# Optimization experiments

Hardware: AMD Instinct MI355X
Metric: run time of the kernel (lower is better)

Reference implementation:

```python
import jax, jax.numpy as jnp
import numpy as np

NUM_EXPERTS = 64
TOP_K = 2
NOISE_STD = 1.0
LOAD_BALANCE_WEIGHT = 0.01
NOISE_KEY = jax.random.fold_in(jax.random.key(0), 12345)


def setup_inputs() -> dict:
    key = jax.random.key(0)
    k1, k2, k3 = jax.random.split(key, 3)
    B, S, D = 4, 4096, 1024
    x = jax.random.normal(k1, (B, S, D), dtype=jnp.float32)
    W_gate = jax.random.normal(k2, (NUM_EXPERTS, D), dtype=jnp.float32) * (1.0 / np.sqrt(D))
    W_noise = jax.random.normal(k3, (NUM_EXPERTS, D), dtype=jnp.float32) * (1.0 / np.sqrt(D))
    return {"x": x, "W_gate": W_gate, "W_noise": W_noise}


def reference(x, W_gate, W_noise):
    # x: [B,S,D], W_gate/W_noise: [E,D] (torch Linear weight layout)
    clean_logits = jnp.einsum("bsd,ed->bse", x, W_gate)           # [B,S,E]
    noise_scale = jax.nn.softplus(jnp.einsum("bsd,ed->bse", x, W_noise))
    noise = jax.random.normal(NOISE_KEY, clean_logits.shape, clean_logits.dtype)
    logits = clean_logits + noise * noise_scale * NOISE_STD

    probs = jax.nn.softmax(logits, axis=-1)                        # [B,S,E]
    routing_weights, expert_indices = jax.lax.top_k(probs, TOP_K)  # [B,S,K]
    routing_weights = routing_weights / jnp.sum(routing_weights, axis=-1, keepdims=True)

    # Load-balance loss on clean logits
    B, S, E = clean_logits.shape
    num_tokens = B * S
    expert_mask = jax.nn.one_hot(expert_indices, E, dtype=jnp.float32).sum(axis=2)  # [B,S,E]
    tokens_per_expert = expert_mask.sum(axis=(0, 1))               # [E]
    fraction_tokens = tokens_per_expert / num_tokens
    router_probs = jax.nn.softmax(clean_logits, axis=-1)
    mean_router_prob = router_probs.mean(axis=(0, 1))              # [E]
    load_balance_loss = LOAD_BALANCE_WEIGHT * E * jnp.sum(fraction_tokens * mean_router_prob)

    noise_scale_mean = noise_scale.mean()
    return (routing_weights, expert_indices, load_balance_loss, router_probs, noise_scale_mean)
```

## Files before the change

kernel.cpp:

```cpp
#include <hip/hip_runtime.h>
#include <stdint.h>

#define TOKENS 16384
#define DDIM   1024
#define NEXP   64
#define NCOL   128
#define TB     32
#define NBLK   (TOKENS / TB)
#define NCH    (DDIM / 32)
#define NTILE  8
#define CPP    8

typedef __attribute__((ext_vector_type(8))) short bf16x8;
typedef __attribute__((ext_vector_type(4))) float f32x4;

__device__ ushort g_wf[3][NTILE][NCH][64][8];
__device__ float g_ps[NEXP];
__device__ float g_cnt[NEXP];
__device__ float g_spa[1];

__device__ inline ushort bf16rne(float f) {
  uint32_t u = __float_as_uint(f);
  return (ushort)((u + 0x7fffu + ((u >> 16) & 1u)) >> 16);
}
__device__ inline float bf16tof(ushort h) {
  return __uint_as_float(((uint32_t)h) << 16);
}
__device__ inline void split3(float v, ushort& h, ushort& m, ushort& l) {
  h = bf16rne(v);
  float r1 = v - bf16tof(h);
  m = bf16rne(r1);
  float r2 = r1 - bf16tof(m);
  l = bf16rne(r2);
}

struct U2 { uint32_t a, b; };

__host__ __device__ constexpr U2 tf2x32(uint32_t k0, uint32_t k1,
                                        uint32_t x0, uint32_t x1) {
  uint32_t ks[3] = {k0, k1, k0 ^ k1 ^ 0x1BD11BDAu};
  const uint32_t rot[2][4] = {{13u, 15u, 26u, 6u}, {17u, 29u, 16u, 24u}};
  x0 += ks[0]; x1 += ks[1];
  for (int d = 0; d < 5; ++d) {
    for (int j = 0; j < 4; ++j) {
      uint32_t r = rot[d & 1][j];
      x0 += x1;
      x1 = (x1 << r) | (x1 >> (32u - r));
      x1 ^= x0;
    }
    x0 += ks[(d + 1) % 3];
    x1 += ks[(d + 2) % 3] + (uint32_t)(d + 1);
  }
  return U2{x0, x1};
}

__device__ inline uint32_t noise_bits(uint32_t i) {
  constexpr U2 NK = tf2x32(0u, 0u, 0u, 12345u);
  U2 o = tf2x32(NK.a, NK.b, 0u, i);
  return o.a ^ o.b;
}

__device__ inline float xla_erfinv(float x) {
  float w = -log1pf(-x * x);
  float p;
  if (w < 5.0f) {
    w = w - 2.5f;
    p = 2.81022636e-08f;
    p = 3.43273939e-07f + p * w;
    p = -3.5233877e-06f + p * w;
    p = -4.39150654e-06f + p * w;
    p = 0.00021858087f + p * w;
    p = -0.00125372503f + p * w;
    p = -0.00417768164f + p * w;
    p = 0.246640727f + p * w;
    p = 1.50140941f + p * w;
  } else {
    w = sqrtf(w) - 3.0f;
    p = -0.000200214257f;
    p = 0.000100950558f + p * w;
    p = 0.00134934322f + p * w;
    p = -0.00367342844f + p * w;
    p = 0.00573950773f + p * w;
    p = -0.0076224613f + p * w;
    p = 0.00943887047f + p * w;
    p = 1.00167406f + p * w;
    p = 2.83297682f + p * w;
  }
  return p * x;
}

__device__ inline float noise_normal(uint32_t i) {
  uint32_t bits = noise_bits(i);
  float f = __uint_as_float((bits >> 9) | 0x3f800000u) - 1.0f;
  float u = f * 2.0f + (-0.99999994f);
  u = fmaxf(u, -0.99999994f);
  return 1.41421356237f * xla_erfinv(u);
}

__device__ inline float softplus_ref(float x) {
  return fmaxf(x, 0.0f) + log1pf(expf(-fabsf(x)));
}

__device__ inline float wave_max64(float v) {
  #pragma unroll
  for (int off = 32; off; off >>= 1) v = fmaxf(v, __shfl_xor(v, off, 64));
  return v;
}
__device__ inline float wave_sum64(float v) {
  #pragma unroll
  for (int off = 32; off; off >>= 1) v += __shfl_xor(v, off, 64);
  return v;
}
__device__ inline void wave_argmax64(float v, int idx, float& mv, int& mi) {
  float bv = v; int bi = idx;
  #pragma unroll
  for (int off = 32; off; off >>= 1) {
    float ov = __shfl_xor(bv, off, 64);
    int   oi = __shfl_xor(bi, off, 64);
    if (ov > bv || (ov == bv && oi < bi)) { bv = ov; bi = oi; }
  }
  mv = bv; mi = bi;
}

__global__ __launch_bounds__(64)
void wsplit_kernel(const float* __restrict__ wg, const float* __restrict__ wn) {
  const int ct   = blockIdx.x >> 5;
  const int kc   = blockIdx.x & 31;
  const int lane = threadIdx.x;
  const int col  = ct * 16 + (lane & 15);
  const int koff = kc * 32 + (lane >> 4) * 8;
  const float* src = (col < NEXP) ? (wg + (size_t)col * DDIM)
                                  : (wn + (size_t)(col - NEXP) * DDIM);
  const float4 v0 = *(const float4*)&src[koff];
  const float4 v1 = *(const float4*)&src[koff + 4];
  const float av[8] = {v0.x, v0.y, v0.z, v0.w, v1.x, v1.y, v1.z, v1.w};
  union BF8 { bf16x8 v; ushort u[8]; };
  BF8 H, M, L;
  #pragma unroll
  for (int j = 0; j < 8; ++j) {
    ushort h, m, l;
    split3(av[j], h, m, l);
    H.u[j] = h; M.u[j] = m; L.u[j] = l;
  }
  *(bf16x8*)&g_wf[0][ct][kc][lane][0] = H.v;
  *(bf16x8*)&g_wf[1][ct][kc][lane][0] = M.v;
  *(bf16x8*)&g_wf[2][ct][kc][lane][0] = L.v;

  if (blockIdx.x == 0) {
    g_ps[lane] = 0.0f; g_cnt[lane] = 0.0f;
    if (lane == 0) g_spa[0] = 0.0f;
  }
}

__global__ __launch_bounds__(512, 4)
void NoisyTopKRouter_57621281243491_kernel(
    const float* __restrict__ x, float* __restrict__ out) {
  __shared__ ushort ldsA[3][2][CPP][64][8];
  __shared__ float lds_logits[TB][NCOL + 4];
  __shared__ float lps[8][NEXP];
  __shared__ float lcb[8][NEXP];
  __shared__ float lspw[8];

  const int tid  = threadIdx.x;
  const int w    = tid >> 6;
  const int lane = tid & 63;
  const int tok0 = blockIdx.x * TB;

  const int srow = tid >> 4;
  const int skq  = tid & 15;
  const int stg  = srow >> 4;
  const int sfr  = srow & 15;
  const int sc   = skq >> 1;
  const int sl0  = ((skq & 1) * 2) * 16 + sfr;
  const int sl1  = ((skq & 1) * 2 + 1) * 16 + sfr;
  const float* sx = x + (size_t)(tok0 + srow) * DDIM + skq * 16;

  const int fr_row = lane & 15;
  const int fr_s   = lane >> 4;
  const ushort* wf = &g_wf[0][0][0][0][0];
  const int b0 = w * 16384 + lane * 8;
  #define PS 131072

  f32x4 acc0 = {0.f, 0.f, 0.f, 0.f};
  f32x4 acc1 = {0.f, 0.f, 0.f, 0.f};

  float4 xrA[4], xrB[4];

  #define SPLIT_PHASE(XR)                                                 \
    {                                                                     \
      union BF8 { bf16x8 v; ushort u[8]; };                               \
      BF8 H0, M0, L0, H1, M1, L1;                                         \
      const float a0v[8] = {XR[0].x, XR[0].y, XR[0].z, XR[0].w,           \
                            XR[1].x, XR[1].y, XR[1].z, XR[1].w};          \
      const float a1v[8] = {XR[2].x, XR[2].y, XR[2].z, XR[2].w,           \
                            XR[3].x, XR[3].y, XR[3].z, XR[3].w};          \
      _Pragma("unroll")                                                   \
      for (int j = 0; j < 8; ++j) {                                       \
        ushort h, m, l;                                                   \
        split3(a0v[j], h, m, l);                                          \
        H0.u[j] = h; M0.u[j] = m; L0.u[j] = l;                            \
        split3(a1v[j], h, m, l);                                          \
        H1.u[j] = h; M1.u[j] = m; L1.u[j] = l;                            \
      }                                                                   \
      *(bf16x8*)&ldsA[0][stg][sc][sl0][0] = H0.v;                         \
      *(bf16x8*)&ldsA[1][stg][sc][sl0][0] = M0.v;                         \
      *(bf16x8*)&ldsA[2][stg][sc][sl0][0] = L0.v;                         \
      *(bf16x8*)&ldsA[0][stg][sc][sl1][0] = H1.v;                         \
      *(bf16x8*)&ldsA[1][stg][sc][sl1][0] = M1.v;                         \
      *(bf16x8*)&ldsA[2][stg][sc][sl1][0] = L1.v;                         \
    }

  #define MFMA_PHASE(ph)                                                  \
    _Pragma("unroll 2")                                                   \
    for (int c = 0; c < CPP; ++c) {                                       \
      const bf16x8 Ah0 = *(const bf16x8*)&ldsA[0][0][c][lane][0];         \
      const bf16x8 Am0 = *(const bf16x8*)&ldsA[1][0][c][lane][0];         \
      const bf16x8 Al0 = *(const bf16x8*)&ldsA[2][0][c][lane][0];         \
      const bf16x8 Ah1 = *(const bf16x8*)&ldsA[0][1][c][lane][0];         \
      const bf16x8 Am1 = *(const bf16x8*)&ldsA[1][1][c][lane][0];         \
      const bf16x8 Al1 = *(const bf16x8*)&ldsA[2][1][c][lane][0];         \
      const int co = ((ph) * CPP + c) * 512;                              \
      const bf16x8 Bh = *(const bf16x8*)&wf[b0 + co];                     \
      const bf16x8 Bm = *(const bf16x8*)&wf[b0 + PS + co];                \
      const bf16x8 Bl = *(const bf16x8*)&wf[b0 + 2 * PS + co];            \
      acc0 = __builtin_amdgcn_mfma_f32_16x16x32_bf16(Ah0, Bh, acc0, 0, 0, 0); \
      acc0 = __builtin_amdgcn_mfma_f32_16x16x32_bf16(Ah0, Bm, acc0, 0, 0, 0); \
      acc0 = __builtin_amdgcn_mfma_f32_16x16x32_bf16(Am0, Bh, acc0, 0, 0, 0); \
      acc0 = __builtin_amdgcn_mfma_f32_16x16x32_bf16(Ah0, Bl, acc0, 0, 0, 0); \
      acc0 = __builtin_amdgcn_mfma_f32_16x16x32_bf16(Al0, Bh, acc0, 0, 0, 0); \
      acc0 = __builtin_amdgcn_mfma_f32_16x16x32_bf16(Am0, Bm, acc0, 0, 0, 0); \
      acc1 = __builtin_amdgcn_mfma_f32_16x16x32_bf16(Ah1, Bh, acc1, 0, 0, 0); \
      acc1 = __builtin_amdgcn_mfma_f32_16x16x32_bf16(Ah1, Bm, acc1, 0, 0, 0); \
      acc1 = __builtin_amdgcn_mfma_f32_16x16x32_bf16(Am1, Bh, acc1, 0, 0, 0); \
      acc1 = __builtin_amdgcn_mfma_f32_16x16x32_bf16(Ah1, Bl, acc1, 0, 0, 0); \
      acc1 = __builtin_amdgcn_mfma_f32_16x16x32_bf16(Al1, Bh, acc1, 0, 0, 0); \
      acc1 = __builtin_amdgcn_mfma_f32_16x16x32_bf16(Am1, Bm, acc1, 0, 0, 0); \
    }

  #pragma unroll
  for (int q = 0; q < 4; ++q) xrA[q] = *(const float4*)&sx[q * 4];

  SPLIT_PHASE(xrA);
  #pragma unroll
  for (int q = 0; q < 4; ++q) xrB[q] = *(const float4*)&sx[256 + q * 4];
  __syncthreads();
  MFMA_PHASE(0);
  __syncthreads();
  SPLIT_PHASE(xrB);
  #pragma unroll
  for (int q = 0; q < 4; ++q) xrA[q] = *(const float4*)&sx[512 + q * 4];
  __syncthreads();
  MFMA_PHASE(1);
  __syncthreads();
  SPLIT_PHASE(xrA);
  #pragma unroll
  for (int q = 0; q < 4; ++q) xrB[q] = *(const float4*)&sx[768 + q * 4];
  __syncthreads();
  MFMA_PHASE(2);
  __syncthreads();
  SPLIT_PHASE(xrB);
  __syncthreads();
  MFMA_PHASE(3);

  #undef SPLIT_PHASE
  #undef MFMA_PHASE
  #undef PS

  #pragma unroll
  for (int r = 0; r < 4; ++r) {
    lds_logits[4 * fr_s + r][w * 16 + fr_row]      = acc0[r];
    lds_logits[16 + 4 * fr_s + r][w * 16 + fr_row] = acc1[r];
  }
  __syncthreads();

  float* out_rw  = out;
  float* out_idx = out + 2 * TOKENS;
  float* out_rp  = out + 4 * TOKENS + 1;

  float ps_acc = 0.0f, sp_acc = 0.0f, c_acc = 0.0f;

  for (int it = 0; it < 4; ++it) {
    const int tl = w * 4 + it;
    const int t  = tok0 + tl;
    const float cl = lds_logits[tl][lane];
    const float nl = lds_logits[tl][NEXP + lane];

    const float m  = wave_max64(cl);
    const float v  = expf(cl - m);
    const float Z  = wave_sum64(v);
    const float rp = v / Z;
    out_rp[(size_t)t * NEXP + lane] = rp;
    ps_acc += rp;

    const float ns  = softplus_ref(nl);
    sp_acc += ns;
    const float noi = noise_normal((uint32_t)(t * NEXP + lane));
    const float lgn = __fadd_rn(cl, __fmul_rn(noi, ns));

    const float m2 = wave_max64(lgn);
    const float v2 = expf(lgn - m2);
    const float Z2 = wave_sum64(v2);
    const float p  = v2 / Z2;

    float p1; int i1;
    wave_argmax64(p, lane, p1, i1);
    const float pm = (lane == i1) ? -3.402823466e38f : p;
    float p2; int i2;
    wave_argmax64(pm, lane, p2, i2);

    c_acc += (float)((lane == i1) + (lane == i2));

    if (lane == 0) {
      const float s = p1 + p2;
      out_rw[t * 2 + 0]  = p1 / s;
      out_rw[t * 2 + 1]  = p2 / s;
      out_idx[t * 2 + 0] = (float)i1;
      out_idx[t * 2 + 1] = (float)i2;
    }
  }

  lps[w][lane] = ps_acc;
  lcb[w][lane] = c_acc;
  const float spw = wave_sum64(sp_acc);
  if (lane == 0) lspw[w] = spw;
  __syncthreads();
  if (tid < NEXP) {
    float a = 0.0f, b = 0.0f;
    #pragma unroll
    for (int j = 0; j < 8; ++j) { a += lps[j][tid]; b += lcb[j][tid]; }
    atomicAdd(&g_ps[tid],  a);
    atomicAdd(&g_cnt[tid], b);
  }
  if (tid == 0) {
    float s = 0.0f;
    #pragma unroll
    for (int j = 0; j < 8; ++j) s += lspw[j];
    atomicAdd(&g_spa[0], s);
  }
}

__global__ void finalize_kernel(float* __restrict__ out) {
  const int lane = threadIdx.x;
  float term = (g_cnt[lane] / (float)TOKENS) * (g_ps[lane] / (float)TOKENS);
  #pragma unroll
  for (int off = 32; off; off >>= 1) term += __shfl_xor(term, off, 64);
  if (lane == 0) {
    out[4 * TOKENS] = 0.64f * term;
    out[4 * TOKENS + 1 + TOKENS * NEXP] = g_spa[0] / (float)(TOKENS * NEXP);
  }
}

extern "C" void kernel_launch(void* const* d_in, const int* in_sizes, int n_in,
                              void* d_out, int out_size, void* d_ws, size_t ws_size,
                              hipStream_t stream) {
  const float* x  = (const float*)d_in[0];
  const float* wg = (const float*)d_in[1];
  const float* wn = (const float*)d_in[2];
  float* out = (float*)d_out;

  (void)d_ws; (void)ws_size; (void)in_sizes; (void)n_in; (void)out_size;

  wsplit_kernel<<<NTILE * NCH, 64, 0, stream>>>(wg, wn);
  NoisyTopKRouter_57621281243491_kernel<<<NBLK, 512, 0, stream>>>(x, out);
  finalize_kernel<<<1, 64, 0, stream>>>(out);
}
```

Before: 144.6 us.

## Halve LDS staging chunk, alias epilogue buffers, swizzle LDS, raise occupancy

Cuts the per-phase K chunk from 8 to 4 MFMA steps and doubles the number of phases from 4 to 8. The logits and reduction scratch buffers now alias the A-staging LDS region, which shrinks shared memory so launch_bounds can ask for 8 blocks per CU. It also adds an XOR swizzle to LDS addresses to avoid bank conflicts. The intent is higher occupancy and fewer LDS conflicts, at the cost of twice as many barriers and smaller per-phase work that hides less latency.

```diff
diff --git a/kernel.cpp b/kernel.cpp
--- a/kernel.cpp
+++ b/kernel.cpp
@@ -9,7 +9,7 @@
 #define NBLK   (TOKENS / TB)
 #define NCH    (DDIM / 32)
 #define NTILE  8
-#define CPP    8
+#define CPP    4
 
 typedef __attribute__((ext_vector_type(8))) short bf16x8;
 typedef __attribute__((ext_vector_type(4))) float f32x4;
@@ -152,28 +152,26 @@
   }
 }
 
-__global__ __launch_bounds__(512, 4)
+__global__ __launch_bounds__(512, 8)
 void NoisyTopKRouter_57621281243491_kernel(
     const float* __restrict__ x, float* __restrict__ out) {
   __shared__ ushort ldsA[3][2][CPP][64][8];
-  __shared__ float lds_logits[TB][NCOL + 4];
-  __shared__ float lps[8][NEXP];
-  __shared__ float lcb[8][NEXP];
-  __shared__ float lspw[8];
 
   const int tid  = threadIdx.x;
   const int w    = tid >> 6;
   const int lane = tid & 63;
   const int tok0 = blockIdx.x * TB;
 
+  char* LA = (char*)&ldsA[0][0][0][0][0];
+
   const int srow = tid >> 4;
   const int skq  = tid & 15;
   const int stg  = srow >> 4;
   const int sfr  = srow & 15;
-  const int sc   = skq >> 1;
-  const int sl0  = ((skq & 1) * 2) * 16 + sfr;
-  const int sl1  = ((skq & 1) * 2 + 1) * 16 + sfr;
-  const float* sx = x + (size_t)(tok0 + srow) * DDIM + skq * 16;
+  const int sc   = skq >> 2;
+  const int ss   = skq & 3;
+  const int so   = (sc * 1024 + ss * 256 + sfr * 16) ^ ((skq & 7) << 4);
+  const float* sx = x + (size_t)(tok0 + srow) * DDIM + skq * 8;
 
   const int fr_row = lane & 15;
   const int fr_s   = lane >> 4;
@@ -184,41 +182,35 @@
   f32x4 acc0 = {0.f, 0.f, 0.f, 0.f};
   f32x4 acc1 = {0.f, 0.f, 0.f, 0.f};
 
-  float4 xrA[4], xrB[4];
-
-  #define SPLIT_PHASE(XR)                                                 \
+  float4 xa0, xa1, xb0, xb1;
+
+  #define SPLIT_PHASE(X0, X1)                                             \
     {                                                                     \
       union BF8 { bf16x8 v; ushort u[8]; };                               \
-      BF8 H0, M0, L0, H1, M1, L1;                                         \
-      const float a0v[8] = {XR[0].x, XR[0].y, XR[0].z, XR[0].w,           \
-                            XR[1].x, XR[1].y, XR[1].z, XR[1].w};          \
-      const float a1v[8] = {XR[2].x, XR[2].y, XR[2].z, XR[2].w,           \
-                            XR[3].x, XR[3].y, XR[3].z, XR[3].w};          \
+      BF8 H, M, L;                                                        \
+      const float av_[8] = {X0.x, X0.y, X0.z, X0.w, X1.x, X1.y, X1.z, X1.w}; \
       _Pragma("unroll")                                                   \
       for (int j = 0; j < 8; ++j) {                                       \
-        ushort h, m, l;                                                   \
-        split3(a0v[j], h, m, l);                                          \
-        H0.u[j] = h; M0.u[j] = m; L0.u[j] = l;                            \
-        split3(a1v[j], h, m, l);                                          \
-        H1.u[j] = h; M1.u[j] = m; L1.u[j] = l;                            \
+        ushort h_, m_, l_;                                                \
+        split3(av_[j], h_, m_, l_);                                       \
+        H.u[j] = h_; M.u[j] = m_; L.u[j] = l_;                            \
       }                                                                   \
-      *(bf16x8*)&ldsA[0][stg][sc][sl0][0] = H0.v;                         \
-      *(bf16x8*)&ldsA[1][stg][sc][sl0][0] = M0.v;                         \
-      *(bf16x8*)&ldsA[2][stg][sc][sl0][0] = L0.v;                         \
-      *(bf16x8*)&ldsA[0][stg][sc][sl1][0] = H1.v;                         \
-      *(bf16x8*)&ldsA[1][stg][sc][sl1][0] = M1.v;                         \
-      *(bf16x8*)&ldsA[2][stg][sc][sl1][0] = L1.v;                         \
+      *(bf16x8*)(LA + stg * 4096 + so)         = H.v;                     \
+      *(bf16x8*)(LA + 8192 + stg * 4096 + so)  = M.v;                     \
+      *(bf16x8*)(LA + 16384 + stg * 4096 + so) = L.v;                     \
     }
 
   #define MFMA_PHASE(ph)                                                  \
-    _Pragma("unroll 2")                                                   \
+    _Pragma("unroll")                                                     \
     for (int c = 0; c < CPP; ++c) {                                       \
-      const bf16x8 Ah0 = *(const bf16x8*)&ldsA[0][0][c][lane][0];         \
-      const bf16x8 Am0 = *(const bf16x8*)&ldsA[1][0][c][lane][0];         \
-      const bf16x8 Al0 = *(const bf16x8*)&ldsA[2][0][c][lane][0];         \
-      const bf16x8 Ah1 = *(const bf16x8*)&ldsA[0][1][c][lane][0];         \
-      const bf16x8 Am1 = *(const bf16x8*)&ldsA[1][1][c][lane][0];         \
-      const bf16x8 Al1 = *(const bf16x8*)&ldsA[2][1][c][lane][0];         \
+      int ro = c * 1024 + lane * 16;                                      \
+      ro ^= ((ro >> 8) & 7) << 4;                                         \
+      const bf16x8 Ah0 = *(const bf16x8*)(LA + ro);                       \
+      const bf16x8 Am0 = *(const bf16x8*)(LA + 8192 + ro);                \
+      const bf16x8 Al0 = *(const bf16x8*)(LA + 16384 + ro);               \
+      const bf16x8 Ah1 = *(const bf16x8*)(LA + 4096 + ro);                \
+      const bf16x8 Am1 = *(const bf16x8*)(LA + 12288 + ro);               \
+      const bf16x8 Al1 = *(const bf16x8*)(LA + 20480 + ro);               \
       const int co = ((ph) * CPP + c) * 512;                              \
       const bf16x8 Bh = *(const bf16x8*)&wf[b0 + co];                     \
       const bf16x8 Bm = *(const bf16x8*)&wf[b0 + PS + co];                \
@@ -237,34 +229,37 @@
       acc1 = __builtin_amdgcn_mfma_f32_16x16x32_bf16(Am1, Bm, acc1, 0, 0, 0); \
     }
 
-  #pragma unroll
-  for (int q = 0; q < 4; ++q) xrA[q] = *(const float4*)&sx[q * 4];
-
-  SPLIT_PHASE(xrA);
-  #pragma unroll
-  for (int q = 0; q < 4; ++q) xrB[q] = *(const float4*)&sx[256 + q * 4];
-  __syncthreads();
-  MFMA_PHASE(0);
-  __syncthreads();
-  SPLIT_PHASE(xrB);
-  #pragma unroll
-  for (int q = 0; q < 4; ++q) xrA[q] = *(const float4*)&sx[512 + q * 4];
-  __syncthreads();
-  MFMA_PHASE(1);
-  __syncthreads();
-  SPLIT_PHASE(xrA);
-  #pragma unroll
-  for (int q = 0; q < 4; ++q) xrB[q] = *(const float4*)&sx[768 + q * 4];
-  __syncthreads();
-  MFMA_PHASE(2);
-  __syncthreads();
-  SPLIT_PHASE(xrB);
-  __syncthreads();
-  MFMA_PHASE(3);
-
+  #define DO_PHASE(ph, C0, C1, N0, N1, PRE)                               \
+    SPLIT_PHASE(C0, C1);                                                  \
+    if (PRE) {                                                            \
+      N0 = *(const float4*)&sx[(ph + 1) * 128];                           \
+      N1 = *(const float4*)&sx[(ph + 1) * 128 + 4];                       \
+    }                                                                     \
+    __syncthreads();                                                      \
+    MFMA_PHASE(ph);                                                       \
+    __syncthreads();
+
+  xa0 = *(const float4*)&sx[0];
+  xa1 = *(const float4*)&sx[4];
+
+  DO_PHASE(0, xa0, xa1, xb0, xb1, 1);
+  DO_PHASE(1, xb0, xb1, xa0, xa1, 1);
+  DO_PHASE(2, xa0, xa1, xb0, xb1, 1);
+  DO_PHASE(3, xb0, xb1, xa0, xa1, 1);
+  DO_PHASE(4, xa0, xa1, xb0, xb1, 1);
+  DO_PHASE(5, xb0, xb1, xa0, xa1, 1);
+  DO_PHASE(6, xa0, xa1, xb0, xb1, 1);
+  DO_PHASE(7, xb0, xb1, xa0, xa1, 0);
+
+  #undef DO_PHASE
   #undef SPLIT_PHASE
   #undef MFMA_PHASE
   #undef PS
+
+  float (*lds_logits)[NCOL + 4] = (float (*)[NCOL + 4])LA;
+  float (*lps)[NEXP] = (float (*)[NEXP])(LA + 16896);
+  float (*lcb)[NEXP] = (float (*)[NEXP])(LA + 18944);
+  float* lspw        = (float*)(LA + 20992);
 
   #pragma unroll
   for (int r = 0; r < 4; ++r) {
```

Result: no change. 143.1 us (-1.1%).
